# Performance work log

Hardware: AMD Instinct MI355X
Metric: run time of the kernel (lower is better)

The kernel has to match this reference:

```python
import jax, jax.numpy as jnp
import numpy as np

B, S, H, NH = 8, 1024, 1024, 16
HD = H // NH


def setup_inputs() -> dict:
    key = jax.random.key(0)
    ks = jax.random.split(key, 9)
    scale = 0.02
    d = {"x": jax.random.normal(ks[0], (B, S, H), jnp.float32)}
    for i, n in enumerate(["q", "k", "v", "o"]):
        d["W" + n] = jax.random.normal(ks[1 + i], (H, H), jnp.float32) * scale
        d["b" + n] = jnp.zeros((H,), jnp.float32)
    d["position_idx"] = jnp.arange(S, dtype=jnp.int32).reshape(1, S)
    return d


def _rotate_half(x):
    x1, x2 = jnp.split(x, 2, axis=-1)
    return jnp.concatenate([-x2, x1], axis=-1)


def _apply_rope(x, position_idx):
    # Faithful to source (precedence bug included): (10000**arange) / head_dim
    inv_freq = 1.0 / (10000.0 ** jnp.arange(0, HD, 2, dtype=jnp.float32) / HD)
    freqs = jnp.einsum('bi,j->bij', position_idx.astype(jnp.float32), inv_freq)  # [1,S,HD/2]
    emb = jnp.concatenate([freqs, freqs], axis=-1)  # [1,S,HD]
    cos = jnp.cos(emb).reshape(1, 1, -1, HD)
    sin = jnp.sin(emb).reshape(1, 1, -1, HD)
    return x * cos + _rotate_half(x) * sin


def reference(x, Wq, bq, Wk, bk, Wv, bv, Wo, bo, position_idx):
    b, s, _ = x.shape

    def to_heads(t):  # [b,s,H] -> [b,nh,s,hd]
        return t.reshape(b, s, NH, HD).transpose(0, 2, 1, 3)

    q = to_heads(x @ Wq + bq)
    k = to_heads(x @ Wk + bk)
    v = to_heads(x @ Wv + bv)
    q = _apply_rope(q, position_idx)
    k = _apply_rope(k, position_idx)
    scores = jnp.einsum('bhqd,bhkd->bhqk', q, k) / jnp.sqrt(jnp.float32(HD))
    attn = jax.nn.softmax(scores, axis=-1)
    out = jnp.einsum('bhqk,bhkd->bhqd', attn, v)  # [b,nh,s,hd]
    out = out.transpose(0, 2, 1, 3).reshape(b, s, NH * HD)
    return out @ Wo + bo
```

## Files before the change

kernel.cpp:

```cpp
#include <hip/hip_runtime.h>
#include <hip/hip_bf16.h>
#include <math.h>

#define B_  8
#define S_  1024
#define H_  1024
#define NH_ 16
#define HD_ 64
#define M_  (B_*S_)
#define K_  1024

typedef __hip_bfloat16 bf16;
typedef __attribute__((ext_vector_type(8))) short  short8;
typedef __attribute__((ext_vector_type(4))) short  short4v;
typedef __attribute__((ext_vector_type(8))) __bf16 bf16x8;
typedef __attribute__((ext_vector_type(4))) float  f32x4;

#define MFMA16(a, b, c) __builtin_amdgcn_mfma_f32_16x16x32_bf16((a), (b), (c), 0, 0, 0)
#define QSCALE 0.18033688011112042f

static __device__ __forceinline__ short f2bf_s(float f) {
  unsigned u = __float_as_uint(f);
  u += 0x7fffu + ((u >> 16) & 1u);
  return (short)(u >> 16);
}
static __device__ __forceinline__ float bf2f_s(short s) {
  return __uint_as_float((unsigned)(unsigned short)s << 16);
}

static __device__ __forceinline__ void gload16(const void* g, void* l) {
  __builtin_amdgcn_global_load_lds(
      (const __attribute__((address_space(1))) void*)g,
      (__attribute__((address_space(3))) void*)l, 16, 0, 0);
}

__global__ __launch_bounds__(256) void convert_x_kernel(const float* __restrict__ x,
                                                        short* __restrict__ xb) {
  int i = blockIdx.x * 256 + threadIdx.x;
  size_t base = (size_t)i * 8;
  f32x4 a = *(const f32x4*)(x + base);
  f32x4 b = *(const f32x4*)(x + base + 4);
  short8 v;
  #pragma unroll
  for (int j = 0; j < 4; ++j) { v[j] = f2bf_s(a[j]); v[4 + j] = f2bf_s(b[j]); }
  *(short8*)(xb + base) = v;
}

__global__ void ingest_bias_kernel(const float* __restrict__ b0, const float* __restrict__ b1,
                                   const float* __restrict__ b2, const float* __restrict__ b3,
                                   short* __restrict__ bbuf) {
  int i = blockIdx.x * 256 + threadIdx.x;
  if (i >= 4096) return;
  const float* src = (i < 1024) ? b0 : (i < 2048) ? b1 : (i < 3072) ? b2 : b3;
  bbuf[i] = f2bf_s(src[i & 1023]);
}

__global__ void rope_tables_kernel(const int* __restrict__ pos,
                                   float* __restrict__ cost, float* __restrict__ sint) {
  int i = blockIdx.x * blockDim.x + threadIdx.x;
  if (i >= S_ * 32) return;
  int s = i >> 5, f = i & 31;
  double inv = 64.0 / pow(10000.0, (double)(2 * f));
  double ang = (double)pos[s] * inv;
  cost[i] = (float)cos(ang);
  sint[i] = (float)sin(ang);
}

__global__ __launch_bounds__(256) void transpose_w_kernel(
    const float* __restrict__ w0, const float* __restrict__ w1,
    const float* __restrict__ w2, const float* __restrict__ w3,
    bf16* __restrict__ outbase) {
  const float* src = (blockIdx.y == 0) ? w0 : (blockIdx.y == 1) ? w1 : (blockIdx.y == 2) ? w2 : w3;
  short* dst = (short*)outbase + (size_t)blockIdx.y * H_ * H_;
  __shared__ short tile[64][72];
  const int t = threadIdx.x;
  const int tr = blockIdx.x >> 4, tc = blockIdx.x & 15;
  const int r0 = tr * 64, c0 = tc * 64;
  #pragma unroll
  for (int p = 0; p < 2; ++p) {
    int row = p * 32 + (t >> 3);
    int c8  = (t & 7) * 8;
    const float* f = src + (size_t)(r0 + row) * H_ + c0 + c8;
    #pragma unroll
    for (int j = 0; j < 8; ++j) tile[c8 + j][row] = f2bf_s(f[j]);
  }
  __syncthreads();
  #pragma unroll
  for (int p = 0; p < 2; ++p) {
    int row = p * 32 + (t >> 3);
    int c8  = (t & 7) * 8;
    short8 v;
    #pragma unroll
    for (int j = 0; j < 8; ++j) v[j] = tile[row][c8 + j];
    *(short8*)(dst + (size_t)(c0 + row) * H_ + r0 + c8) = v;
  }
}

__global__ __launch_bounds__(256) void gemm_bt_kernel(
    const bf16* __restrict__ A, const bf16* __restrict__ Bt, const short* __restrict__ bias,
    void* __restrict__ C, const float* __restrict__ cost, const float* __restrict__ sint,
    int mode, float qscale) {
  __shared__ short sA[128 * 64];
  __shared__ short sB[128 * 64];
  const int t  = threadIdx.x;
  const int bm = blockIdx.y * 128, bn = blockIdx.x * 128;
  const int lane = t & 63, wid = t >> 6;
  const int wr = wid >> 1, wc = wid & 1;
  const int lm = lane & 15, lg = lane >> 4;
  f32x4 acc[4][4] = {};

  const short* Ag = (const short*)A;
  const short* Bg = (const short*)Bt;

  for (int k0 = 0; k0 < K_; k0 += 64) {
    #pragma unroll
    for (int c = 0; c < 4; ++c) {
      int flat = c * 256 + t;
      int row = flat >> 3, cc = flat & 7;
      int gcol = (cc ^ (row & 7)) * 8;
      gload16(Ag + (size_t)(bm + row) * K_ + k0 + gcol, sA + flat * 8);
      gload16(Bg + (size_t)(bn + row) * K_ + k0 + gcol, sB + flat * 8);
    }
    __syncthreads();
    #pragma unroll
    for (int kk2 = 0; kk2 < 2; ++kk2) {
      bf16x8 af[4], bfr[4];
      #pragma unroll
      for (int i = 0; i < 4; ++i) {
        int row = wr * 64 + i * 16 + lm;
        af[i] = *(const bf16x8*)(sA + row * 64 + (((kk2 << 2) + lg) ^ (row & 7)) * 8);
      }
      #pragma unroll
      for (int j = 0; j < 4; ++j) {
        int row = wc * 64 + j * 16 + lm;
        bfr[j] = *(const bf16x8*)(sB + row * 64 + (((kk2 << 2) + lg) ^ (row & 7)) * 8);
      }
      #pragma unroll
      for (int i = 0; i < 4; ++i)
        #pragma unroll
        for (int j = 0; j < 4; ++j)
          acc[i][j] = MFMA16(af[i], bfr[j], acc[i][j]);
    }
    __syncthreads();
  }

  if (mode == 0) {
    #pragma unroll
    for (int i = 0; i < 4; ++i) {
      int row = bm + wr * 64 + i * 16 + lg * 4;
      #pragma unroll
      for (int j = 0; j < 4; ++j) {
        int col = bn + wc * 64 + j * 16 + lm;
        float bv = bf2f_s(bias[col]);
        #pragma unroll
        for (int r = 0; r < 4; ++r)
          ((float*)C)[(size_t)(row + r) * H_ + col] = acc[i][j][r] + bv;
      }
    }
  } else if (mode == 1) {
    #pragma unroll
    for (int i = 0; i < 4; ++i) {
      int row = bm + wr * 64 + i * 16 + lg * 4;
      #pragma unroll
      for (int j = 0; j < 2; ++j) {
        int col0 = bn + wc * 64 + j * 16 + lm;
        int d = col0 & 63;
        float b0 = bf2f_s(bias[col0]);
        float b1 = bf2f_s(bias[col0 + 32]);
        #pragma unroll
        for (int r = 0; r < 4; ++r) {
          int s = (row + r) & (S_ - 1);
          float cv = cost[s * 32 + d] * qscale, sv = sint[s * 32 + d] * qscale;
          float x1 = acc[i][j][r] + b0;
          float x2 = acc[i][j + 2][r] + b1;
          ((short*)C)[(size_t)(row + r) * H_ + col0]      = f2bf_s(x1 * cv - x2 * sv);
          ((short*)C)[(size_t)(row + r) * H_ + col0 + 32] = f2bf_s(x2 * cv + x1 * sv);
        }
      }
    }
  } else {
    #pragma unroll
    for (int i = 0; i < 4; ++i) {
      int row = bm + wr * 64 + i * 16 + lg * 4;
      int bb = row >> 10;
      int sb = row & 1023;
      int pos = (sb & ~31) | (((sb >> 2) & 3) << 3) | (((sb >> 4) & 1) << 2);
      #pragma unroll
      for (int j = 0; j < 4; ++j) {
        int col = bn + wc * 64 + j * 16 + lm;
        int colv = col & 1023;
        float bv = bf2f_s(bias[col]);
        short4v pk;
        #pragma unroll
        for (int r = 0; r < 4; ++r) pk[r] = f2bf_s(acc[i][j][r] + bv);
        short* dstp = (short*)C + ((size_t)(bb * NH_ + (colv >> 6)) * HD_ + (colv & 63)) * S_ + pos;
        *(short4v*)dstp = pk;
      }
    }
  }
}

__global__ __launch_bounds__(256) void attn_kernel(
    const bf16* __restrict__ q, const bf16* __restrict__ k,
    const bf16* __restrict__ vt, bf16* __restrict__ o) {
  const int bh = blockIdx.x, b = bh >> 4, h = bh & 15;
  const int t = threadIdx.x, wid = t >> 6, lane = t & 63;
  const int lm = lane & 15, lg = lane >> 4;
  const int qw = blockIdx.y * 256 + wid * 64;

  __shared__ short sK[2][32 * 64];
  __shared__ short sV[2][64 * 32];

  const int keyr = t >> 3, ccK = t & 7, tcK = ccK ^ (keyr & 7);
  const int dr   = t >> 2, ccV = t & 3, tcV = ccV ^ (dr & 3);
  const short* ksrc = (const short*)k + (size_t)(b * S_ + keyr) * H_ + h * HD_ + tcK * 8;
  const short* vsrc = (const short*)vt + (size_t)bh * HD_ * S_ + (size_t)dr * S_ + tcV * 8;

  const int kO0 = lm * 64 + ((lg ^ (lm & 7)) << 3);
  const int kO1 = lm * 64 + (((4 + lg) ^ (lm & 7)) << 3);
  const int vO  = lm * 32 + ((lg ^ (lm & 3)) << 3);

  const short* qbase = (const short*)q + (size_t)(b * S_ + qw) * H_ + h * HD_;
  bf16x8 qf[4][2];
  #pragma unroll
  for (int mi = 0; mi < 4; ++mi)
    #pragma unroll
    for (int dh = 0; dh < 2; ++dh)
      qf[mi][dh] = *(const bf16x8*)(qbase + (size_t)(mi * 16 + lm) * H_ + dh * 32 + lg * 8);

  float ps[4] = {};
  f32x4 oacc[4][4] = {};

  gload16(ksrc, sK[0] + t * 8);
  gload16(vsrc, sV[0] + t * 8);
  __syncthreads();

  int cur = 0;
  for (int kk = 0; kk < S_; kk += 32) {
    if (kk + 32 < S_) {
      gload16(ksrc + (size_t)(kk + 32) * H_, sK[cur ^ 1] + t * 8);
      gload16(vsrc + (kk + 32), sV[cur ^ 1] + t * 8);
    }
    const short* sKc = sK[cur];
    const short* sVc = sV[cur];

    f32x4 sc[4][2];
    #pragma unroll
    for (int nt = 0; nt < 2; ++nt) {
      bf16x8 kf0 = *(const bf16x8*)(sKc + nt * 16 * 64 + kO0);
      bf16x8 kf1 = *(const bf16x8*)(sKc + nt * 16 * 64 + kO1);
      #pragma unroll
      for (int mi = 0; mi < 4; ++mi) {
        f32x4 z = {};
        z = MFMA16(kf0, qf[mi][0], z);
        sc[mi][nt] = MFMA16(kf1, qf[mi][1], z);
      }
    }
    bf16x8 vf[4];
    #pragma unroll
    for (int dt = 0; dt < 4; ++dt)
      vf[dt] = *(const bf16x8*)(sVc + dt * 16 * 32 + vO);

    bf16x8 pf[4];
    #pragma unroll
    for (int mi = 0; mi < 4; ++mi)
      #pragma unroll
      for (int nt = 0; nt < 2; ++nt)
        #pragma unroll
        for (int r = 0; r < 4; ++r) {
          float p = exp2f(sc[mi][nt][r]);
          ps[mi] += p;
          pf[mi][nt * 4 + r] = (__bf16)p;
        }
    #pragma unroll
    for (int mi = 0; mi < 4; ++mi)
      #pragma unroll
      for (int dt = 0; dt < 4; ++dt)
        oacc[mi][dt] = MFMA16(pf[mi], vf[dt], oacc[mi][dt]);

    __syncthreads();
    cur ^= 1;
  }
  #pragma unroll
  for (int mi = 0; mi < 4; ++mi) {
    ps[mi] += __shfl_xor(ps[mi], 16);
    ps[mi] += __shfl_xor(ps[mi], 32);
  }
  #pragma unroll
  for (int mi = 0; mi < 4; ++mi) {
    #pragma unroll
    for (int r = 0; r < 4; ++r) {
      float rr = 1.0f / __shfl(ps[mi], lg * 4 + r);
      int row = qw + mi * 16 + lg * 4 + r;
      #pragma unroll
      for (int dt = 0; dt < 4; ++dt) {
        int col = h * HD_ + dt * 16 + lm;
        ((short*)o)[(size_t)(b * S_ + row) * H_ + col] = f2bf_s(oacc[mi][dt][r] * rr);
      }
    }
  }
}

extern "C" void kernel_launch(void* const* d_in, const int* in_sizes, int n_in,
                              void* d_out, int out_size, void* d_ws, size_t ws_size,
                              hipStream_t stream) {
  (void)out_size; (void)ws_size;
  int ix, iWq, iWk, iWv, iWo, ibq, ibk, ibv, ibo, ipos;
  const int XS = 8388608, WS = 1048576;
  if (n_in == 10 && in_sizes[0] == WS && in_sizes[9] == XS) {
    iWk = 0; iWo = 1; iWq = 2; iWv = 3; ibk = 4; ibo = 5; ibq = 6; ibv = 7; ipos = 8; ix = 9;
  } else if (n_in == 10 && in_sizes[0] == 1024 && in_sizes[9] == XS) {
    ipos = 0; ibo = 1; iWo = 2; ibv = 3; iWv = 4; ibk = 5; iWk = 6; ibq = 7; iWq = 8; ix = 9;
  } else if (n_in == 10 && in_sizes[0] == XS && in_sizes[1] == 1024) {
    ix = 0; ipos = 1; ibv = 2; ibq = 3; ibo = 4; ibk = 5; iWv = 6; iWq = 7; iWo = 8; iWk = 9;
  } else {
    ix = 0; iWq = 1; ibq = 2; iWk = 3; ibk = 4; iWv = 5; ibv = 6; iWo = 7; ibo = 8; ipos = 9;
  }
  const float* x  = (const float*)d_in[ix];
  const float* Wq = (const float*)d_in[iWq];
  const float* bq = (const float*)d_in[ibq];
  const float* Wk = (const float*)d_in[iWk];
  const float* bk = (const float*)d_in[ibk];
  const float* Wv = (const float*)d_in[iWv];
  const float* bv = (const float*)d_in[ibv];
  const float* Wo = (const float*)d_in[iWo];
  const float* bo = (const float*)d_in[ibo];
  const int*  pos = (const int*)d_in[ipos];

  char* ws = (char*)d_ws;
  bf16* wt    = (bf16*)(ws);
  bf16* kb    = (bf16*)(ws + (8ull  << 20));
  bf16* vtb   = (bf16*)(ws + (24ull << 20));
  bf16* obuf  = (bf16*)(ws + (40ull << 20));
  float* cost = (float*)(ws + (40ull << 20));
  float* sint = (float*)(ws + (40ull << 20) + (size_t)S_ * 32 * sizeof(float));
  short* bbuf = (short*)(ws + (56ull << 20));
  bf16* qb    = (bf16*)d_out;
  short* xb   = (short*)((char*)d_out + (16ull << 20));

  const int NEL = H_ * H_;
  rope_tables_kernel<<<dim3(128), 256, 0, stream>>>(pos, cost, sint);
  ingest_bias_kernel<<<dim3(16), 256, 0, stream>>>(bq, bk, bv, bo, bbuf);
  transpose_w_kernel<<<dim3(256, 4), 256, 0, stream>>>(Wq, Wk, Wv, Wo, wt);
  convert_x_kernel<<<dim3(4096), 256, 0, stream>>>(x, xb);
  gemm_bt_kernel<<<dim3(8, 64), 256, 0, stream>>>((const bf16*)xb, wt + 0 * NEL, bbuf + 0,
                                                  qb,  cost, sint, 1, QSCALE);
  gemm_bt_kernel<<<dim3(8, 64), 256, 0, stream>>>((const bf16*)xb, wt + 1 * NEL, bbuf + 1024,
                                                  kb,  cost, sint, 1, 1.0f);
  gemm_bt_kernel<<<dim3(8, 64), 256, 0, stream>>>((const bf16*)xb, wt + 2 * NEL, bbuf + 2048,
                                                  vtb, cost, sint, 2, 1.0f);
  attn_kernel<<<dim3(128, 4), 256, 0, stream>>>(qb, kb, vtb, obuf);
  gemm_bt_kernel<<<dim3(8, 64), 256, 0, stream>>>(obuf, wt + 3 * NEL, bbuf + 3072,
                                                  d_out, cost, sint, 0, 1.0f);
}
```

Measured before the change: 187.3 us.

## Double-buffer GEMM shared tiles and widen attention key block to 64

The projection GEMM now keeps two LDS buffers for its A and B tiles and prefetches the next K-slice while MFMAs run on the current one, which removes one barrier per iteration and overlaps global loads with compute. The attention kernel processes 64 keys per iteration instead of 32, so half as many loop iterations and barriers are needed, with a larger K/V tile loaded per step. The cost is twice the LDS in the GEMM (64KB) and attention, plus more registers for score and fragment arrays, which may lower occupancy.

```diff
diff --git a/kernel.cpp b/kernel.cpp
--- a/kernel.cpp
+++ b/kernel.cpp
@@ -100,8 +100,8 @@
     const bf16* __restrict__ A, const bf16* __restrict__ Bt, const short* __restrict__ bias,
     void* __restrict__ C, const float* __restrict__ cost, const float* __restrict__ sint,
     int mode, float qscale) {
-  __shared__ short sA[128 * 64];
-  __shared__ short sB[128 * 64];
+  __shared__ short sA[2][128 * 64];
+  __shared__ short sB[2][128 * 64];
   const int t  = threadIdx.x;
   const int bm = blockIdx.y * 128, bn = blockIdx.x * 128;
   const int lane = t & 63, wid = t >> 6;
@@ -112,28 +112,42 @@
   const short* Ag = (const short*)A;
   const short* Bg = (const short*)Bt;
 
+  #pragma unroll
+  for (int c = 0; c < 4; ++c) {
+    int flat = c * 256 + t;
+    int row = flat >> 3, cc = flat & 7;
+    int gcol = (cc ^ (row & 7)) * 8;
+    gload16(Ag + (size_t)(bm + row) * K_ + gcol, sA[0] + flat * 8);
+    gload16(Bg + (size_t)(bn + row) * K_ + gcol, sB[0] + flat * 8);
+  }
+  __syncthreads();
+
+  int cur = 0;
   for (int k0 = 0; k0 < K_; k0 += 64) {
-    #pragma unroll
-    for (int c = 0; c < 4; ++c) {
-      int flat = c * 256 + t;
-      int row = flat >> 3, cc = flat & 7;
-      int gcol = (cc ^ (row & 7)) * 8;
-      gload16(Ag + (size_t)(bm + row) * K_ + k0 + gcol, sA + flat * 8);
-      gload16(Bg + (size_t)(bn + row) * K_ + k0 + gcol, sB + flat * 8);
-    }
-    __syncthreads();
+    if (k0 + 64 < K_) {
+      #pragma unroll
+      for (int c = 0; c < 4; ++c) {
+        int flat = c * 256 + t;
+        int row = flat >> 3, cc = flat & 7;
+        int gcol = (cc ^ (row & 7)) * 8;
+        gload16(Ag + (size_t)(bm + row) * K_ + k0 + 64 + gcol, sA[cur ^ 1] + flat * 8);
+        gload16(Bg + (size_t)(bn + row) * K_ + k0 + 64 + gcol, sB[cur ^ 1] + flat * 8);
+      }
+    }
+    const short* sAc = sA[cur];
+    const short* sBc = sB[cur];
     #pragma unroll
     for (int kk2 = 0; kk2 < 2; ++kk2) {
       bf16x8 af[4], bfr[4];
       #pragma unroll
       for (int i = 0; i < 4; ++i) {
         int row = wr * 64 + i * 16 + lm;
-        af[i] = *(const bf16x8*)(sA + row * 64 + (((kk2 << 2) + lg) ^ (row & 7)) * 8);
+        af[i] = *(const bf16x8*)(sAc + row * 64 + (((kk2 << 2) + lg) ^ (row & 7)) * 8);
       }
       #pragma unroll
       for (int j = 0; j < 4; ++j) {
         int row = wc * 64 + j * 16 + lm;
-        bfr[j] = *(const bf16x8*)(sB + row * 64 + (((kk2 << 2) + lg) ^ (row & 7)) * 8);
+        bfr[j] = *(const bf16x8*)(sBc + row * 64 + (((kk2 << 2) + lg) ^ (row & 7)) * 8);
       }
       #pragma unroll
       for (int i = 0; i < 4; ++i)
@@ -142,6 +156,7 @@
           acc[i][j] = MFMA16(af[i], bfr[j], acc[i][j]);
     }
     __syncthreads();
+    cur ^= 1;
   }
 
   if (mode == 0) {
@@ -208,17 +223,18 @@
   const int lm = lane & 15, lg = lane >> 4;
   const int qw = blockIdx.y * 256 + wid * 64;
 
-  __shared__ short sK[2][32 * 64];
-  __shared__ short sV[2][64 * 32];
-
-  const int keyr = t >> 3, ccK = t & 7, tcK = ccK ^ (keyr & 7);
-  const int dr   = t >> 2, ccV = t & 3, tcV = ccV ^ (dr & 3);
-  const short* ksrc = (const short*)k + (size_t)(b * S_ + keyr) * H_ + h * HD_ + tcK * 8;
-  const short* vsrc = (const short*)vt + (size_t)bh * HD_ * S_ + (size_t)dr * S_ + tcV * 8;
-
-  const int kO0 = lm * 64 + ((lg ^ (lm & 7)) << 3);
-  const int kO1 = lm * 64 + (((4 + lg) ^ (lm & 7)) << 3);
-  const int vO  = lm * 32 + ((lg ^ (lm & 3)) << 3);
+  __shared__ short sK[2][64 * 64];
+  __shared__ short sV[2][64 * 64];
+
+  const int r0 = t >> 3, cc = t & 7;
+  const int swz = (cc ^ (r0 & 7)) * 8;
+  const short* ksrc0 = (const short*)k + (size_t)(b * S_ + r0) * H_ + h * HD_ + swz;
+  const short* ksrc1 = ksrc0 + 32 * H_;
+  const short* vsrc0 = (const short*)vt + (size_t)bh * HD_ * S_ + (size_t)r0 * S_ + swz;
+  const short* vsrc1 = vsrc0 + 32 * S_;
+
+  const int fO0 = lm * 64 + ((lg ^ (lm & 7)) << 3);
+  const int fO1 = lm * 64 + (((4 + lg) ^ (lm & 7)) << 3);
 
   const short* qbase = (const short*)q + (size_t)(b * S_ + qw) * H_ + h * HD_;
   bf16x8 qf[4][2];
@@ -231,52 +247,62 @@
   float ps[4] = {};
   f32x4 oacc[4][4] = {};
 
-  gload16(ksrc, sK[0] + t * 8);
-  gload16(vsrc, sV[0] + t * 8);
+  gload16(ksrc0, sK[0] + t * 8);
+  gload16(ksrc1, sK[0] + (256 + t) * 8);
+  gload16(vsrc0, sV[0] + t * 8);
+  gload16(vsrc1, sV[0] + (256 + t) * 8);
   __syncthreads();
 
   int cur = 0;
-  for (int kk = 0; kk < S_; kk += 32) {
-    if (kk + 32 < S_) {
-      gload16(ksrc + (size_t)(kk + 32) * H_, sK[cur ^ 1] + t * 8);
-      gload16(vsrc + (kk + 32), sV[cur ^ 1] + t * 8);
+  for (int kk = 0; kk < S_; kk += 64) {
+    if (kk + 64 < S_) {
+      gload16(ksrc0 + (size_t)(kk + 64) * H_, sK[cur ^ 1] + t * 8);
+      gload16(ksrc1 + (size_t)(kk + 64) * H_, sK[cur ^ 1] + (256 + t) * 8);
+      gload16(vsrc0 + (kk + 64), sV[cur ^ 1] + t * 8);
+      gload16(vsrc1 + (kk + 64), sV[cur ^ 1] + (256 + t) * 8);
     }
     const short* sKc = sK[cur];
     const short* sVc = sV[cur];
 
-    f32x4 sc[4][2];
-    #pragma unroll
-    for (int nt = 0; nt < 2; ++nt) {
-      bf16x8 kf0 = *(const bf16x8*)(sKc + nt * 16 * 64 + kO0);
-      bf16x8 kf1 = *(const bf16x8*)(sKc + nt * 16 * 64 + kO1);
-      #pragma unroll
-      for (int mi = 0; mi < 4; ++mi) {
+    bf16x8 kf[4][2];
+    #pragma unroll
+    for (int nt = 0; nt < 4; ++nt) {
+      kf[nt][0] = *(const bf16x8*)(sKc + nt * 16 * 64 + fO0);
+      kf[nt][1] = *(const bf16x8*)(sKc + nt * 16 * 64 + fO1);
+    }
+    f32x4 sc[4][4];
+    #pragma unroll
+    for (int mi = 0; mi < 4; ++mi)
+      #pragma unroll
+      for (int nt = 0; nt < 4; ++nt) {
         f32x4 z = {};
-        z = MFMA16(kf0, qf[mi][0], z);
-        sc[mi][nt] = MFMA16(kf1, qf[mi][1], z);
-      }
-    }
-    bf16x8 vf[4];
-    #pragma unroll
-    for (int dt = 0; dt < 4; ++dt)
-      vf[dt] = *(const bf16x8*)(sVc + dt * 16 * 32 + vO);
-
-    bf16x8 pf[4];
+        z = MFMA16(kf[nt][0], qf[mi][0], z);
+        sc[mi][nt] = MFMA16(kf[nt][1], qf[mi][1], z);
+      }
+    bf16x8 vf[2][4];
+    #pragma unroll
+    for (int dt = 0; dt < 4; ++dt) {
+      vf[0][dt] = *(const bf16x8*)(sVc + dt * 16 * 64 + fO0);
+      vf[1][dt] = *(const bf16x8*)(sVc + dt * 16 * 64 + fO1);
+    }
+    bf16x8 pf[4][2];
     #pragma unroll
     for (int mi = 0; mi < 4; ++mi)
       #pragma unroll
-      for (int nt = 0; nt < 2; ++nt)
-        #pragma unroll
-        for (int r = 0; r < 4; ++r) {
-          float p = exp2f(sc[mi][nt][r]);
+      for (int ks = 0; ks < 2; ++ks)
+        #pragma unroll
+        for (int j = 0; j < 8; ++j) {
+          float p = exp2f(sc[mi][ks * 2 + (j >> 2)][j & 3]);
           ps[mi] += p;
-          pf[mi][nt * 4 + r] = (__bf16)p;
+          pf[mi][ks][j] = (__bf16)p;
         }
     #pragma unroll
-    for (int mi = 0; mi < 4; ++mi)
-      #pragma unroll
-      for (int dt = 0; dt < 4; ++dt)
-        oacc[mi][dt] = MFMA16(pf[mi], vf[dt], oacc[mi][dt]);
+    for (int ks = 0; ks < 2; ++ks)
+      #pragma unroll
+      for (int mi = 0; mi < 4; ++mi)
+        #pragma unroll
+        for (int dt = 0; dt < 4; ++dt)
+          oacc[mi][dt] = MFMA16(pf[mi][ks], vf[ks][dt], oacc[mi][dt]);
 
     __syncthreads();
     cur ^= 1;
```

After: 203.6 us. 1.09x slower.
